# Kernel tuning notes

Measured on AMD Instinct MI355X. Metric: run time of the kernel, lower is better.

Reference implementation:

```python
import jax, jax.numpy as jnp
import numpy as np
from jax import lax

FIRE_RATE = 0.5       # forward() default fire_rate
INPUT_CHANNELS = 1    # module input_channels
EPS = 1e-5            # BatchNorm eps


def p4_conv_z2(x, w, b):
    """Z2 -> P4 group conv. x: [B,I,H,W], w: [O,I,k,k] -> [B,O,4,H,W]."""
    # rotate the spatial kernel by r*90deg for each of the 4 output orientations
    ws = jnp.stack([jnp.rot90(w, r, axes=(2, 3)) for r in range(4)], axis=1)  # [O,4,I,k,k]
    O, _, I, k, _ = ws.shape
    y = lax.conv_general_dilated(x, ws.reshape(O * 4, I, k, k), (1, 1), 'SAME',
                                 dimension_numbers=('NCHW', 'OIHW', 'NCHW'))
    B, _, H, W = x.shape
    return y.reshape(B, O, 4, H, W) + b[None, :, None, None, None]


def p4_conv_p4(x, w, b):
    """P4 -> P4 group conv. x: [B,I,4,H,W], w: [O,I,4,k,k] -> [B,O,4,H,W]."""
    # for output orientation r: cyclic-shift input-orientation axis by r and rotate spatially by r
    ws = jnp.stack([jnp.rot90(jnp.roll(w, r, axis=2), r, axes=(3, 4)) for r in range(4)],
                   axis=1)  # [O,4,I,4,k,k]
    O, _, I, _, k, _ = ws.shape
    B, _, _, H, W = x.shape
    y = lax.conv_general_dilated(x.reshape(B, I * 4, H, W),
                                 ws.reshape(O * 4, I * 4, k, k), (1, 1), 'SAME',
                                 dimension_numbers=('NCHW', 'OIHW', 'NCHW'))
    return y.reshape(B, O, 4, H, W) + b[None, :, None, None, None]


def _update(x_nhwc, w1, b1, gamma, beta, w2, b2, key):
    x = jnp.transpose(x_nhwc, (0, 3, 1, 2))            # [B,C,H,W]
    y = p4_conv_z2(x, w1, b1)                          # [B,Ch,4,H,W]
    # BatchNorm3d (batch stats, affine): normalize each channel over (B, rot, H, W)
    mu = jnp.mean(y, axis=(0, 2, 3, 4), keepdims=True)
    var = jnp.var(y, axis=(0, 2, 3, 4), keepdims=True)
    y = gamma[None, :, None, None, None] * (y - mu) * lax.rsqrt(var + EPS) \
        + beta[None, :, None, None, None]
    y = jax.nn.relu(y)
    dy = p4_conv_p4(y, w2, b2).mean(axis=2)            # mean over rotation axis -> [B,C,H,W]
    B, _, H, W = dy.shape
    mask = (jax.random.uniform(key, (B, 1, H, W), dtype=dy.dtype) > FIRE_RATE).astype(dy.dtype)
    x = x + dy * mask
    return jnp.transpose(x, (0, 2, 3, 1))              # back to [B,H,W,C]


def nca_forward(x, w1, b1, gamma, beta, w2, b2, steps):
    base_key = jax.random.key(42)
    for step in range(steps):
        x2 = _update(x, w1, b1, gamma, beta, w2, b2, jax.random.fold_in(base_key, step))
        # first input_channels are clamped to the original input
        x = jnp.concatenate((x[..., :INPUT_CHANNELS], x2[..., INPUT_CHANNELS:]), axis=-1)
    return x


def setup_inputs() -> dict:
    key = jax.random.key(0)
    ks = jax.random.split(key, 6)
    B, H, W = 8, 192, 192
    C = 16            # channel_n
    CH = 128 // 8     # base_hidden_size = hidden_size // 8
    K = 7             # kernel_size
    # fan-in scaled init (matches nn.Conv2d-style scaling)
    x = jax.random.normal(ks[0], (B, H, W, C), dtype=jnp.float32)
    w1 = jax.random.normal(ks[1], (CH, C, K, K), dtype=jnp.float32) / np.sqrt(C * K * K)
    b1 = jnp.zeros((CH,), dtype=jnp.float32)
    gamma = jnp.ones((CH,), dtype=jnp.float32)
    beta = jnp.zeros((CH,), dtype=jnp.float32)
    w2 = jax.random.normal(ks[2], (C, CH, 4, 1, 1), dtype=jnp.float32) / np.sqrt(CH * 4)
    b2 = jnp.zeros((C,), dtype=jnp.float32)
    return {"x": x, "w1": w1, "b1": b1, "gamma": gamma, "beta": beta,
            "w2": w2, "b2": b2, "steps": 10}


def reference(x, w1, b1, gamma, beta, w2, b2, steps):
    return nca_forward(x, w1, b1, gamma, beta, w2, b2, steps)
```

## Files before the change

### kernel.cpp

```cpp
#include <hip/hip_runtime.h>
#include <stdint.h>

#define HH 192
#define WW 192
#define BB 8
#define NSTEP 10
#define HWSZ (HH*WW)
#define NPIX (BB*HWSZ)
#define TILE 16

#define XROWS 23
#define RSU   376
#define XBUFU (XROWS*RSU)
#define NKS   25

typedef _Float16 f16x8 __attribute__((ext_vector_type(8)));
typedef float    f32x4 __attribute__((ext_vector_type(4)));

union PackU { ushort u[8]; uint4 v; };

__host__ __device__ inline void tf2x32(uint32_t k0, uint32_t k1,
                                       uint32_t x0, uint32_t x1,
                                       uint32_t &o0, uint32_t &o1) {
  const uint32_t k2 = k0 ^ k1 ^ 0x1BD11BDAu;
  x0 += k0; x1 += k1;
#define TFR(r) { x0 += x1; x1 = (x1 << (r)) | (x1 >> (32 - (r))); x1 ^= x0; }
  TFR(13) TFR(15) TFR(26) TFR(6)
  x0 += k1; x1 += k2 + 1u;
  TFR(17) TFR(29) TFR(16) TFR(24)
  x0 += k2; x1 += k0 + 2u;
  TFR(13) TFR(15) TFR(26) TFR(6)
  x0 += k0; x1 += k1 + 3u;
  TFR(17) TFR(29) TFR(16) TFR(24)
  x0 += k1; x1 += k2 + 4u;
  TFR(13) TFR(15) TFR(26) TFR(6)
  x0 += k2; x1 += k0 + 5u;
#undef TFR
  o0 = x0; o1 = x1;
}

__device__ inline void split2048(float v, ushort &h, ushort &l) {
  _Float16 hi = (_Float16)v;
  float r = (v - (float)hi) * 2048.0f;
  _Float16 lo = (_Float16)r;
  h = __builtin_bit_cast(ushort, hi);
  l = __builtin_bit_cast(ushort, lo);
}

__global__ void k_prep_wfrag(const float* __restrict__ w1,
                             ushort* __restrict__ wfh, ushort* __restrict__ wfl) {
  int idx = blockIdx.x * 256 + threadIdx.x;
  if (idx >= NKS * 4 * 64) return;
  const int lane = idx & 63;
  const int sm = idx >> 6;
  const int s = sm >> 2, mt = sm & 3;
  const int m = lane & 15, g = lane >> 4;
  const int j = mt * 16 + m, co = j >> 2, r = j & 3;
  const int t = 2 * s + (g >> 1);
  PackU ph, pl;
#pragma unroll
  for (int e = 0; e < 8; ++e) {
    const int ci = 8 * (g & 1) + e;
    float wv = 0.f;
    if (t < 49) {
      const int ky = t / 7, kx = t - (t / 7) * 7;
      int a = ky, b = kx;
      for (int i = 0; i < r; ++i) { int na = b, nb = 6 - a; a = na; b = nb; }
      wv = w1[((co * 16 + ci) * 7 + a) * 7 + b];
    }
    split2048(wv, ph.u[e], pl.u[e]);
  }
  ((uint4*)wfh)[sm * 64 + lane] = ph.v;
  ((uint4*)wfl)[sm * 64 + lane] = pl.v;
}

__global__ void k_prep_w2(const float* __restrict__ w2, float* __restrict__ wsum) {
  int idx = threadIdx.x;
  float s = 0.f;
  for (int t = 0; t < 4; ++t) s += w2[idx * 4 + t];
  wsum[idx] = 0.25f * s;
}

__global__ __launch_bounds__(512) void k_conv1(
    const float* __restrict__ xsrc,
    const ushort* __restrict__ wfh,
    const ushort* __restrict__ wfl,
    const float* __restrict__ b1,
    float* __restrict__ y,
    float* __restrict__ partials)
{
  __shared__ __align__(16) ushort xs[2 * XBUFU];
  __shared__ float red2[8][32];
  const int tid = threadIdx.x;
  const int lane = tid & 63, wid = tid >> 6;
  const int x0 = blockIdx.x * TILE, y0 = blockIdx.y * TILE;
  const int b = blockIdx.z;

  for (int p = tid; p < XROWS * 22; p += 512) {
    const int lr = p / 22, lc = p - (p / 22) * 22;
    const int gy = y0 + lr - 3, gx = x0 + lc - 3;
    float4 v0, v1, v2, v3;
    if ((unsigned)gy < (unsigned)HH && (unsigned)gx < (unsigned)WW) {
      const float4* px = (const float4*)(xsrc + ((size_t)b * HWSZ + (size_t)gy * WW + gx) * 16);
      v0 = px[0]; v1 = px[1]; v2 = px[2]; v3 = px[3];
    } else {
      v0 = v1 = v2 = v3 = make_float4(0.f, 0.f, 0.f, 0.f);
    }
    const float xv[16] = {v0.x, v0.y, v0.z, v0.w, v1.x, v1.y, v1.z, v1.w,
                          v2.x, v2.y, v2.z, v2.w, v3.x, v3.y, v3.z, v3.w};
    PackU h0, h1, l0, l1;
#pragma unroll
    for (int c = 0; c < 8; ++c) split2048(xv[c], h0.u[c], l0.u[c]);
#pragma unroll
    for (int c = 0; c < 8; ++c) split2048(xv[8 + c], h1.u[c], l1.u[c]);
    const int ub = lr * RSU + lc * 16;
    *(uint4*)&xs[ub] = h0.v;
    *(uint4*)&xs[ub + 8] = h1.v;
    *(uint4*)&xs[XBUFU + ub] = l0.v;
    *(uint4*)&xs[XBUFU + ub + 8] = l1.v;
  }
  __syncthreads();

  const int n = lane & 15;
  const int q = lane >> 4;
  const int h = q & 1;
  const int c0 = 2 * wid;
  const int bU0 = n * RSU + c0 * 16 + h * 8;
  const int bU1 = bU0 + 16;

  const f16x8* __restrict__ WAh = (const f16x8*)wfh;
  const f16x8* __restrict__ WAl = (const f16x8*)wfl;

  float bias[4];
#pragma unroll
  for (int mt = 0; mt < 4; ++mt) bias[mt] = b1[mt * 4 + q];

  f32x4 accH[2][4], accC[2][4];
#pragma unroll
  for (int st = 0; st < 2; ++st)
#pragma unroll
    for (int mt = 0; mt < 4; ++mt) {
      const float bv = bias[mt];
      accH[st][mt] = (f32x4){bv, bv, bv, bv};
      accC[st][mt] = (f32x4){0.f, 0.f, 0.f, 0.f};
    }

  f16x8 Ah[2][4], Al[2][4];
  f16x8 Bh0[2], Bl0[2], Bh1[2], Bl1[2];

#pragma unroll
  for (int mt = 0; mt < 4; ++mt) {
    Ah[0][mt] = WAh[mt * 64 + lane];
    Al[0][mt] = WAl[mt * 64 + lane];
  }
  {
    const int off = (lane < 32) ? 0 : 16;
    Bh0[0] = *(const f16x8*)&xs[bU0 + off];
    Bl0[0] = *(const f16x8*)&xs[XBUFU + bU0 + off];
    Bh1[0] = *(const f16x8*)&xs[bU1 + off];
    Bl1[0] = *(const f16x8*)&xs[XBUFU + bU1 + off];
  }

#pragma unroll
  for (int s = 0; s < NKS; ++s) {
    const int cb = s & 1, nb = cb ^ 1;
    if (s < NKS - 1) {
#pragma unroll
      for (int mt = 0; mt < 4; ++mt) {
        const int f = ((s + 1) * 4 + mt) * 64 + lane;
        Ah[nb][mt] = WAh[f];
        Al[nb][mt] = WAl[f];
      }
      const int t0 = 2 * (s + 1), t1 = t0 + 1;
      const int o0 = (t0 / 7) * RSU + (t0 % 7) * 16;
      const int o1 = (t1 < 49) ? (t1 / 7) * RSU + (t1 % 7) * 16 : 0;
      const int off = (lane < 32) ? o0 : o1;
      Bh0[nb] = *(const f16x8*)&xs[bU0 + off];
      Bl0[nb] = *(const f16x8*)&xs[XBUFU + bU0 + off];
      Bh1[nb] = *(const f16x8*)&xs[bU1 + off];
      Bl1[nb] = *(const f16x8*)&xs[XBUFU + bU1 + off];
    }
    __builtin_amdgcn_sched_barrier(0);
    __builtin_amdgcn_s_setprio(1);
#pragma unroll
    for (int mt = 0; mt < 4; ++mt) {
      accH[0][mt] = __builtin_amdgcn_mfma_f32_16x16x32_f16(Ah[cb][mt], Bh0[cb], accH[0][mt], 0, 0, 0);
      accH[1][mt] = __builtin_amdgcn_mfma_f32_16x16x32_f16(Ah[cb][mt], Bh1[cb], accH[1][mt], 0, 0, 0);
      accC[0][mt] = __builtin_amdgcn_mfma_f32_16x16x32_f16(Ah[cb][mt], Bl0[cb], accC[0][mt], 0, 0, 0);
      accC[0][mt] = __builtin_amdgcn_mfma_f32_16x16x32_f16(Al[cb][mt], Bh0[cb], accC[0][mt], 0, 0, 0);
      accC[1][mt] = __builtin_amdgcn_mfma_f32_16x16x32_f16(Ah[cb][mt], Bl1[cb], accC[1][mt], 0, 0, 0);
      accC[1][mt] = __builtin_amdgcn_mfma_f32_16x16x32_f16(Al[cb][mt], Bh1[cb], accC[1][mt], 0, 0, 0);
    }
    __builtin_amdgcn_s_setprio(0);
    __builtin_amdgcn_sched_barrier(0);
  }

  float sC[4] = {0.f, 0.f, 0.f, 0.f}, qC[4] = {0.f, 0.f, 0.f, 0.f};
#pragma unroll
  for (int st = 0; st < 2; ++st) {
    const size_t pix = (size_t)b * HWSZ + (size_t)(y0 + n) * WW + (x0 + c0 + st);
#pragma unroll
    for (int mt = 0; mt < 4; ++mt) {
      f32x4 res = accH[st][mt] + accC[st][mt] * 4.8828125e-4f;
      *(float4*)(y + pix * 64 + mt * 16 + q * 4) =
          make_float4(res[0], res[1], res[2], res[3]);
#pragma unroll
      for (int r = 0; r < 4; ++r) { sC[mt] += res[r]; qC[mt] += res[r] * res[r]; }
    }
  }
#pragma unroll
  for (int mt = 0; mt < 4; ++mt) {
    float s = sC[mt], s2 = qC[mt];
#pragma unroll
    for (int off = 1; off <= 8; off <<= 1) {
      s += __shfl_xor(s, off); s2 += __shfl_xor(s2, off);
    }
    if (n == 0) {
      red2[wid][(mt * 4 + q) * 2] = s;
      red2[wid][(mt * 4 + q) * 2 + 1] = s2;
    }
  }
  __syncthreads();
  if (tid < 32) {
    float v = 0.f;
#pragma unroll
    for (int w2i = 0; w2i < 8; ++w2i) v += red2[w2i][tid];
    const int blk = (b * gridDim.y + blockIdx.y) * gridDim.x + blockIdx.x;
    partials[(size_t)blk * 32 + tid] = v;
  }
}

__global__ __launch_bounds__(256) void k_bnstats(
    const float* __restrict__ partials,
    const float* __restrict__ gamma, const float* __restrict__ beta,
    float* __restrict__ stats)
{
  const int c = blockIdx.x;
  const int tid = threadIdx.x;
  float s = 0.f, s2 = 0.f;
  for (int i = tid; i < 1152; i += 256) {
    s  += partials[(size_t)i * 32 + 2 * c];
    s2 += partials[(size_t)i * 32 + 2 * c + 1];
  }
  __shared__ float rs[256], rs2[256];
  rs[tid] = s; rs2[tid] = s2;
  __syncthreads();
  for (int off = 128; off > 0; off >>= 1) {
    if (tid < off) { rs[tid] += rs[tid + off]; rs2[tid] += rs2[tid + off]; }
    __syncthreads();
  }
  if (tid == 0) {
    const float N = (float)BB * 4.f * HH * WW;
    const float mu = rs[0] / N;
    const float var = rs2[0] / N - mu * mu;
    const float rstd = rsqrtf(var + 1e-5f);
    const float sc = gamma[c] * rstd;
    stats[2 * c]     = sc;
    stats[2 * c + 1] = beta[c] - mu * sc;
  }
}

__global__ __launch_bounds__(256) void k_update(
    const float* __restrict__ xsrc,
    const float* __restrict__ y,
    const float* __restrict__ stats,
    const float* __restrict__ wsum,
    const float* __restrict__ b2,
    float* __restrict__ xdst,
    uint32_t fk0, uint32_t fk1)
{
  __shared__ float sss[32];
  __shared__ float sws[256];
  __shared__ float sb2[16];
  const int tid = threadIdx.x;
  sws[tid] = wsum[tid];
  if (tid < 32) sss[tid] = stats[tid];
  if (tid < 16) sb2[tid] = b2[tid];
  __syncthreads();

  const size_t pix = (size_t)blockIdx.x * 256 + tid;
  const float4* yp = (const float4*)(y + pix * 64);
  float ysum[16];
#pragma unroll
  for (int c = 0; c < 16; ++c) {
    const float4 v = yp[c];
    const float sc = sss[2 * c], sh = sss[2 * c + 1];
    ysum[c] = fmaxf(fmaf(sc, v.x, sh), 0.f) + fmaxf(fmaf(sc, v.y, sh), 0.f)
            + fmaxf(fmaf(sc, v.z, sh), 0.f) + fmaxf(fmaf(sc, v.w, sh), 0.f);
  }

  uint32_t h0, h1;
  tf2x32(fk0, fk1, 0u, (uint32_t)pix, h0, h1);
  const uint32_t bits = h0 ^ h1;
  const float u = __uint_as_float((bits >> 9) | 0x3f800000u) - 1.0f;
  const float m = (u > 0.5f) ? 1.0f : 0.0f;

  const float4* xp = (const float4*)(xsrc + pix * 16);
  float4* op = (float4*)(xdst + pix * 16);
#pragma unroll
  for (int qq = 0; qq < 4; ++qq) {
    const float4 xv = xp[qq];
    float d[4];
#pragma unroll
    for (int jj = 0; jj < 4; ++jj) {
      const int o = 4 * qq + jj;
      float s = sb2[o];
#pragma unroll
      for (int c = 0; c < 16; ++c) s = fmaf(sws[o * 16 + c], ysum[c], s);
      d[jj] = s;
    }
    float4 r;
    r.x = xv.x + d[0] * m;
    r.y = xv.y + d[1] * m;
    r.z = xv.z + d[2] * m;
    r.w = xv.w + d[3] * m;
    if (qq == 0) r.x = xv.x;
    op[qq] = r;
  }
}

extern "C" void kernel_launch(void* const* d_in, const int* in_sizes, int n_in,
                              void* d_out, int out_size, void* d_ws, size_t ws_size,
                              hipStream_t stream) {
  const float* x_in  = (const float*)d_in[0];
  const float* w1    = (const float*)d_in[1];
  const float* b1    = (const float*)d_in[2];
  const float* gamma = (const float*)d_in[3];
  const float* beta  = (const float*)d_in[4];
  const float* w2    = (const float*)d_in[5];
  const float* b2    = (const float*)d_in[6];
  float* out = (float*)d_out;

  float* ws       = (float*)d_ws;
  float* y        = ws;
  ushort* wfh     = (ushort*)(y + (size_t)NPIX * 64);
  ushort* wfl     = wfh + NKS * 4 * 64 * 8;
  float* wsum     = (float*)(wfl + NKS * 4 * 64 * 8);
  float* partials = wsum + 256;
  float* stats    = partials + 1152 * 32;

  k_prep_wfrag<<<NKS, 256, 0, stream>>>(w1, wfh, wfl);
  k_prep_w2<<<1, 256, 0, stream>>>(w2, wsum);

  for (int s = 0; s < NSTEP; ++s) {
    const float* xsrc = (s == 0) ? x_in : out;
    k_conv1<<<dim3(WW / TILE, HH / TILE, BB), 512, 0, stream>>>(xsrc, wfh, wfl, b1, y, partials);
    k_bnstats<<<16, 256, 0, stream>>>(partials, gamma, beta, stats);
    uint32_t fk0, fk1;
    tf2x32(0u, 42u, 0u, (uint32_t)s, fk0, fk1);
    k_update<<<NPIX / 256, 256, 0, stream>>>(xsrc, y, stats, wsum, b2, out, fk0, fk1);
  }
}
```

Before: 1.236 ms.

## Widen conv tiles, stage weight fragments via LDS async loads, fold BN stats into update

The conv tile grows to 24x16 so each wave computes three pixel columns instead of two, which increases reuse of each weight fragment. Weight fragments now go from global to LDS with global_load_lds, double-buffered, with a block-wide barrier at every step. The separate BN-stats kernel is removed, and every update block re-reduces the 768 partials itself. This saves one launch per step, but each update block now repeats that partials read, and the extra per-step barriers could stall the MFMA pipeline.

Measured after the change: 1.293 ms. +4.6%, slower.

```diff
diff --git a/kernel.cpp b/kernel.cpp
--- a/kernel.cpp
+++ b/kernel.cpp
@@ -7,15 +7,20 @@
 #define NSTEP 10
 #define HWSZ (HH*WW)
 #define NPIX (BB*HWSZ)
-#define TILE 16
-
-#define XROWS 23
-#define RSU   376
+#define TILE_W 24
+#define TILE_H 16
+#define XROWS 22
+#define XCOLS 30
+#define RSU   488
 #define XBUFU (XROWS*RSU)
 #define NKS   25
+#define NBLK  (8*12*8)
 
 typedef _Float16 f16x8 __attribute__((ext_vector_type(8)));
 typedef float    f32x4 __attribute__((ext_vector_type(4)));
+
+typedef __attribute__((address_space(1))) const uint32_t glb_u32;
+typedef __attribute__((address_space(3))) uint32_t lds_u32;
 
 union PackU { ushort u[8]; uint4 v; };
 
@@ -81,7 +86,7 @@
   wsum[idx] = 0.25f * s;
 }
 
-__global__ __launch_bounds__(512) void k_conv1(
+__global__ __launch_bounds__(512, 2) void k_conv1(
     const float* __restrict__ xsrc,
     const ushort* __restrict__ wfh,
     const ushort* __restrict__ wfl,
@@ -89,55 +94,56 @@
     float* __restrict__ y,
     float* __restrict__ partials)
 {
-  __shared__ __align__(16) ushort xs[2 * XBUFU];
+  __shared__ __align__(16) ushort xsm[2 * XBUFU];
+  __shared__ __align__(16) ushort abh[2][2048];
+  __shared__ __align__(16) ushort abl[2][2048];
   __shared__ float red2[8][32];
   const int tid = threadIdx.x;
   const int lane = tid & 63, wid = tid >> 6;
-  const int x0 = blockIdx.x * TILE, y0 = blockIdx.y * TILE;
+  const int x0 = blockIdx.x * TILE_W, y0 = blockIdx.y * TILE_H;
   const int b = blockIdx.z;
 
-  for (int p = tid; p < XROWS * 22; p += 512) {
-    const int lr = p / 22, lc = p - (p / 22) * 22;
+  {
+    const ushort* gsrc = ((wid < 4) ? wfh : wfl) + (wid & 3) * 512 + lane * 8;
+    ushort* ldst = ((wid < 4) ? abh[0] : abl[0]) + (wid & 3) * 512;
+    __builtin_amdgcn_global_load_lds((glb_u32*)gsrc, (lds_u32*)ldst, 16, 0, 0);
+  }
+
+  for (int p = tid; p < XROWS * XCOLS * 2; p += 512) {
+    const int half = p & 1, t2 = p >> 1;
+    const int lr = t2 / XCOLS, lc = t2 - (t2 / XCOLS) * XCOLS;
     const int gy = y0 + lr - 3, gx = x0 + lc - 3;
-    float4 v0, v1, v2, v3;
+    float4 v0, v1;
     if ((unsigned)gy < (unsigned)HH && (unsigned)gx < (unsigned)WW) {
-      const float4* px = (const float4*)(xsrc + ((size_t)b * HWSZ + (size_t)gy * WW + gx) * 16);
-      v0 = px[0]; v1 = px[1]; v2 = px[2]; v3 = px[3];
+      const float4* px = (const float4*)(xsrc + ((size_t)b * HWSZ + (size_t)gy * WW + gx) * 16 + half * 8);
+      v0 = px[0]; v1 = px[1];
     } else {
-      v0 = v1 = v2 = v3 = make_float4(0.f, 0.f, 0.f, 0.f);
-    }
-    const float xv[16] = {v0.x, v0.y, v0.z, v0.w, v1.x, v1.y, v1.z, v1.w,
-                          v2.x, v2.y, v2.z, v2.w, v3.x, v3.y, v3.z, v3.w};
-    PackU h0, h1, l0, l1;
-#pragma unroll
-    for (int c = 0; c < 8; ++c) split2048(xv[c], h0.u[c], l0.u[c]);
-#pragma unroll
-    for (int c = 0; c < 8; ++c) split2048(xv[8 + c], h1.u[c], l1.u[c]);
-    const int ub = lr * RSU + lc * 16;
-    *(uint4*)&xs[ub] = h0.v;
-    *(uint4*)&xs[ub + 8] = h1.v;
-    *(uint4*)&xs[XBUFU + ub] = l0.v;
-    *(uint4*)&xs[XBUFU + ub + 8] = l1.v;
+      v0 = v1 = make_float4(0.f, 0.f, 0.f, 0.f);
+    }
+    const float xv[8] = {v0.x, v0.y, v0.z, v0.w, v1.x, v1.y, v1.z, v1.w};
+    PackU h, l;
+#pragma unroll
+    for (int c = 0; c < 8; ++c) split2048(xv[c], h.u[c], l.u[c]);
+    const int ub = lr * RSU + lc * 16 + half * 8;
+    *(uint4*)&xsm[ub] = h.v;
+    *(uint4*)&xsm[XBUFU + ub] = l.v;
   }
   __syncthreads();
 
   const int n = lane & 15;
   const int q = lane >> 4;
   const int h = q & 1;
-  const int c0 = 2 * wid;
-  const int bU0 = n * RSU + c0 * 16 + h * 8;
+  const int bU0 = n * RSU + (3 * wid + 0) * 16 + h * 8;
   const int bU1 = bU0 + 16;
-
-  const f16x8* __restrict__ WAh = (const f16x8*)wfh;
-  const f16x8* __restrict__ WAl = (const f16x8*)wfl;
+  const int bU2 = bU0 + 32;
 
   float bias[4];
 #pragma unroll
   for (int mt = 0; mt < 4; ++mt) bias[mt] = b1[mt * 4 + q];
 
-  f32x4 accH[2][4], accC[2][4];
-#pragma unroll
-  for (int st = 0; st < 2; ++st)
+  f32x4 accH[3][4], accC[3][4];
+#pragma unroll
+  for (int st = 0; st < 3; ++st)
 #pragma unroll
     for (int mt = 0; mt < 4; ++mt) {
       const float bv = bias[mt];
@@ -145,60 +151,68 @@
       accC[st][mt] = (f32x4){0.f, 0.f, 0.f, 0.f};
     }
 
-  f16x8 Ah[2][4], Al[2][4];
-  f16x8 Bh0[2], Bl0[2], Bh1[2], Bl1[2];
-
-#pragma unroll
-  for (int mt = 0; mt < 4; ++mt) {
-    Ah[0][mt] = WAh[mt * 64 + lane];
-    Al[0][mt] = WAl[mt * 64 + lane];
-  }
+  f16x8 Ah[4], Al[4];
+  f16x8 Bh[2][3], Bl[2][3];
+
   {
     const int off = (lane < 32) ? 0 : 16;
-    Bh0[0] = *(const f16x8*)&xs[bU0 + off];
-    Bl0[0] = *(const f16x8*)&xs[XBUFU + bU0 + off];
-    Bh1[0] = *(const f16x8*)&xs[bU1 + off];
-    Bl1[0] = *(const f16x8*)&xs[XBUFU + bU1 + off];
+    Bh[0][0] = *(const f16x8*)&xsm[bU0 + off];
+    Bl[0][0] = *(const f16x8*)&xsm[XBUFU + bU0 + off];
+    Bh[0][1] = *(const f16x8*)&xsm[bU1 + off];
+    Bl[0][1] = *(const f16x8*)&xsm[XBUFU + bU1 + off];
+    Bh[0][2] = *(const f16x8*)&xsm[bU2 + off];
+    Bl[0][2] = *(const f16x8*)&xsm[XBUFU + bU2 + off];
   }
 
 #pragma unroll
   for (int s = 0; s < NKS; ++s) {
     const int cb = s & 1, nb = cb ^ 1;
     if (s < NKS - 1) {
-#pragma unroll
-      for (int mt = 0; mt < 4; ++mt) {
-        const int f = ((s + 1) * 4 + mt) * 64 + lane;
-        Ah[nb][mt] = WAh[f];
-        Al[nb][mt] = WAl[f];
-      }
+      const ushort* gsrc = ((wid < 4) ? wfh : wfl) + (s + 1) * 2048 + (wid & 3) * 512 + lane * 8;
+      ushort* ldst = ((wid < 4) ? abh[nb] : abl[nb]) + (wid & 3) * 512;
+      __builtin_amdgcn_global_load_lds((glb_u32*)gsrc, (lds_u32*)ldst, 16, 0, 0);
+    }
+#pragma unroll
+    for (int mt = 0; mt < 4; ++mt) Ah[mt] = *(const f16x8*)&abh[cb][mt * 512 + lane * 8];
+#pragma unroll
+    for (int mt = 0; mt < 4; ++mt) Al[mt] = *(const f16x8*)&abl[cb][mt * 512 + lane * 8];
+    if (s < NKS - 1) {
       const int t0 = 2 * (s + 1), t1 = t0 + 1;
       const int o0 = (t0 / 7) * RSU + (t0 % 7) * 16;
       const int o1 = (t1 < 49) ? (t1 / 7) * RSU + (t1 % 7) * 16 : 0;
       const int off = (lane < 32) ? o0 : o1;
-      Bh0[nb] = *(const f16x8*)&xs[bU0 + off];
-      Bl0[nb] = *(const f16x8*)&xs[XBUFU + bU0 + off];
-      Bh1[nb] = *(const f16x8*)&xs[bU1 + off];
-      Bl1[nb] = *(const f16x8*)&xs[XBUFU + bU1 + off];
+      Bh[nb][0] = *(const f16x8*)&xsm[bU0 + off];
+      Bl[nb][0] = *(const f16x8*)&xsm[XBUFU + bU0 + off];
+      Bh[nb][1] = *(const f16x8*)&xsm[bU1 + off];
+      Bl[nb][1] = *(const f16x8*)&xsm[XBUFU + bU1 + off];
+      Bh[nb][2] = *(const f16x8*)&xsm[bU2 + off];
+      Bl[nb][2] = *(const f16x8*)&xsm[XBUFU + bU2 + off];
     }
     __builtin_amdgcn_sched_barrier(0);
     __builtin_amdgcn_s_setprio(1);
 #pragma unroll
     for (int mt = 0; mt < 4; ++mt) {
-      accH[0][mt] = __builtin_amdgcn_mfma_f32_16x16x32_f16(Ah[cb][mt], Bh0[cb], accH[0][mt], 0, 0, 0);
-      accH[1][mt] = __builtin_amdgcn_mfma_f32_16x16x32_f16(Ah[cb][mt], Bh1[cb], accH[1][mt], 0, 0, 0);
-      accC[0][mt] = __builtin_amdgcn_mfma_f32_16x16x32_f16(Ah[cb][mt], Bl0[cb], accC[0][mt], 0, 0, 0);
-      accC[0][mt] = __builtin_amdgcn_mfma_f32_16x16x32_f16(Al[cb][mt], Bh0[cb], accC[0][mt], 0, 0, 0);
-      accC[1][mt] = __builtin_amdgcn_mfma_f32_16x16x32_f16(Ah[cb][mt], Bl1[cb], accC[1][mt], 0, 0, 0);
-      accC[1][mt] = __builtin_amdgcn_mfma_f32_16x16x32_f16(Al[cb][mt], Bh1[cb], accC[1][mt], 0, 0, 0);
+#pragma unroll
+      for (int st = 0; st < 3; ++st)
+        accH[st][mt] = __builtin_amdgcn_mfma_f32_16x16x32_f16(Ah[mt], Bh[cb][st], accH[st][mt], 0, 0, 0);
+    }
+#pragma unroll
+    for (int mt = 0; mt < 4; ++mt) {
+#pragma unroll
+      for (int st = 0; st < 3; ++st) {
+        accC[st][mt] = __builtin_amdgcn_mfma_f32_16x16x32_f16(Ah[mt], Bl[cb][st], accC[st][mt], 0, 0, 0);
+        accC[st][mt] = __builtin_amdgcn_mfma_f32_16x16x32_f16(Al[mt], Bh[cb][st], accC[st][mt], 0, 0, 0);
+      }
     }
     __builtin_amdgcn_s_setprio(0);
     __builtin_amdgcn_sched_barrier(0);
+    __syncthreads();
   }
 
   float sC[4] = {0.f, 0.f, 0.f, 0.f}, qC[4] = {0.f, 0.f, 0.f, 0.f};
 #pragma unroll
-  for (int st = 0; st < 2; ++st) {
-    const size_t pix = (size_t)b * HWSZ + (size_t)(y0 + n) * WW + (x0 + c0 + st);
+  for (int st = 0; st < 3; ++st) {
+    const size_t pix = (size_t)b * HWSZ + (size_t)(y0 + n) * WW + (x0 + 3 * wid + st);
 #pragma unroll
     for (int mt = 0; mt < 4; ++mt) {
       f32x4 res = accH[st][mt] + accC[st][mt] * 4.8828125e-4f;
@@ -230,52 +244,42 @@
   }
 }
 
-__global__ __launch_bounds__(256) void k_bnstats(
-    const float* __restrict__ partials,
-    const float* __restrict__ gamma, const float* __restrict__ beta,
-    float* __restrict__ stats)
-{
-  const int c = blockIdx.x;
-  const int tid = threadIdx.x;
-  float s = 0.f, s2 = 0.f;
-  for (int i = tid; i < 1152; i += 256) {
-    s  += partials[(size_t)i * 32 + 2 * c];
-    s2 += partials[(size_t)i * 32 + 2 * c + 1];
-  }
-  __shared__ float rs[256], rs2[256];
-  rs[tid] = s; rs2[tid] = s2;
-  __syncthreads();
-  for (int off = 128; off > 0; off >>= 1) {
-    if (tid < off) { rs[tid] += rs[tid + off]; rs2[tid] += rs2[tid + off]; }
-    __syncthreads();
-  }
-  if (tid == 0) {
-    const float N = (float)BB * 4.f * HH * WW;
-    const float mu = rs[0] / N;
-    const float var = rs2[0] / N - mu * mu;
-    const float rstd = rsqrtf(var + 1e-5f);
-    const float sc = gamma[c] * rstd;
-    stats[2 * c]     = sc;
-    stats[2 * c + 1] = beta[c] - mu * sc;
-  }
-}
-
 __global__ __launch_bounds__(256) void k_update(
     const float* __restrict__ xsrc,
     const float* __restrict__ y,
-    const float* __restrict__ stats,
+    const float* __restrict__ partials,
+    const float* __restrict__ gamma, const float* __restrict__ beta,
     const float* __restrict__ wsum,
     const float* __restrict__ b2,
     float* __restrict__ xdst,
     uint32_t fk0, uint32_t fk1)
 {
+  __shared__ float redp[8][32];
   __shared__ float sss[32];
   __shared__ float sws[256];
   __shared__ float sb2[16];
   const int tid = threadIdx.x;
   sws[tid] = wsum[tid];
-  if (tid < 32) sss[tid] = stats[tid];
   if (tid < 16) sb2[tid] = b2[tid];
+
+  {
+    const int j = tid & 31, g = tid >> 5;
+    float s = 0.f;
+    for (int i = g; i < NBLK; i += 8) s += partials[(size_t)i * 32 + j];
+    redp[g][j] = s;
+  }
+  __syncthreads();
+  if (tid < 16) {
+    float s1 = 0.f, s2 = 0.f;
+#pragma unroll
+    for (int g = 0; g < 8; ++g) { s1 += redp[g][2 * tid]; s2 += redp[g][2 * tid + 1]; }
+    const float N = (float)BB * 4.f * HH * WW;
+    const float mu = s1 / N;
+    const float var = s2 / N - mu * mu;
+    const float sc = gamma[tid] * rsqrtf(var + 1e-5f);
+    sss[2 * tid]     = sc;
+    sss[2 * tid + 1] = beta[tid] - mu * sc;
+  }
   __syncthreads();
 
   const size_t pix = (size_t)blockIdx.x * 256 + tid;
@@ -334,20 +338,18 @@
   float* ws       = (float*)d_ws;
   float* y        = ws;
   ushort* wfh     = (ushort*)(y + (size_t)NPIX * 64);
-  ushort* wfl     = wfh + NKS * 4 * 64 * 8;
-  float* wsum     = (float*)(wfl + NKS * 4 * 64 * 8);
+  ushort* wfl     = wfh + NKS * 2048;
+  float* wsum     = (float*)(wfl + NKS * 2048);
   float* partials = wsum + 256;
-  float* stats    = partials + 1152 * 32;
 
   k_prep_wfrag<<<NKS, 256, 0, stream>>>(w1, wfh, wfl);
   k_prep_w2<<<1, 256, 0, stream>>>(w2, wsum);
 
   for (int s = 0; s < NSTEP; ++s) {
     const float* xsrc = (s == 0) ? x_in : out;
-    k_conv1<<<dim3(WW / TILE, HH / TILE, BB), 512, 0, stream>>>(xsrc, wfh, wfl, b1, y, partials);
-    k_bnstats<<<16, 256, 0, stream>>>(partials, gamma, beta, stats);
+    k_conv1<<<dim3(WW / TILE_W, HH / TILE_H, BB), 512, 0, stream>>>(xsrc, wfh, wfl, b1, y, partials);
     uint32_t fk0, fk1;
     tf2x32(0u, 42u, 0u, (uint32_t)s, fk0, fk1);
-    k_update<<<NPIX / 256, 256, 0, stream>>>(xsrc, y, stats, wsum, b2, out, fk0, fk1);
-  }
-}
+    k_update<<<NPIX / 256, 256, 0, stream>>>(xsrc, y, partials, gamma, beta, wsum, b2, out, fk0, fk1);
+  }
+}
```
